# Kernel tuning notes

Hardware: AMD Instinct MI355X
Metric: run time of the kernel (lower is better)

## Reference

```python
import math
import jax, jax.numpy as jnp
import numpy as np

NUM_HEADS = 12
NUM_LANDMARKS = 32

def iterative_inv(mat, n_iter=6):
    # mat: [B, H, m, m] row-stochastic kernel; Newton-Schulz pseudo-inverse
    m = mat.shape[-1]
    I = jnp.eye(m, dtype=mat.dtype)
    K = mat
    # 'else' branch: per-(B,H) normalization by max column sum
    denom = jnp.max(jnp.sum(K, axis=-2), axis=-1)[..., None, None]
    V = jnp.swapaxes(K, -1, -2) / denom
    for _ in range(n_iter):
        KV = jnp.matmul(K, V)
        V = jnp.matmul(0.25 * V, 13.0 * I - jnp.matmul(KV, 15.0 * I - jnp.matmul(KV, 7.0 * I - KV)))
    return V

def setup_inputs() -> dict:
    key = jax.random.key(0)
    k1, k2, k3 = jax.random.split(key, 3)
    B, N, C = 8, 2048, 768
    x = jax.random.normal(k1, (B, N, C), dtype=jnp.float32)
    w_qkv = jax.random.normal(k2, (C, 3 * C), dtype=jnp.float32) * (1.0 / math.sqrt(C))
    w_proj = jax.random.normal(k3, (C, C), dtype=jnp.float32) * (1.0 / math.sqrt(C))
    b_proj = jnp.zeros((C,), dtype=jnp.float32)
    return {"x": x, "w_qkv": w_qkv, "w_proj": w_proj, "b_proj": b_proj}

def reference(x, w_qkv, w_proj, b_proj):
    B, N, C = x.shape
    H = NUM_HEADS
    d = C // H
    m = NUM_LANDMARKS
    qkv = (x @ w_qkv).reshape(B, N, 3, H, d).transpose(2, 0, 3, 1, 4)  # [3,B,H,N,d]
    Q, K, V = qkv[0], qkv[1], qkv[2]
    scale = 1.0 / math.sqrt(math.sqrt(d))
    Q = Q * scale
    K = K * scale
    # landmark pooling: mean over contiguous chunks of size N//m
    Q_l = Q.reshape(B, H, m, N // m, d).mean(axis=-2)  # [B,H,m,d]
    K_l = K.reshape(B, H, m, N // m, d).mean(axis=-2)
    kernel_1 = jax.nn.softmax(jnp.einsum('bhnd,bhmd->bhnm', Q, K_l), axis=-1)   # [B,H,N,m]
    kernel_2 = jax.nn.softmax(jnp.einsum('bhmd,bhkd->bhmk', Q_l, K_l), axis=-1) # [B,H,m,m]
    kernel_3 = jax.nn.softmax(jnp.einsum('bhmd,bhnd->bhmn', Q_l, K), axis=-1)   # [B,H,m,N]
    X = jnp.matmul(jnp.matmul(kernel_1, iterative_inv(kernel_2)), jnp.matmul(kernel_3, V))  # [B,H,N,d]
    X = X.transpose(0, 2, 1, 3).reshape(B, N, C)
    return X @ w_proj + b_proj
```

## Files before the change

### kernel.cpp

```cpp
#include <hip/hip_runtime.h>
#include <hip/hip_bf16.h>

typedef __hip_bfloat16 bf16;
typedef __attribute__((ext_vector_type(8))) __bf16 bf16x8;
typedef __attribute__((ext_vector_type(4))) float f32x4;

#define NB 8
#define SEQ 2048
#define CH 768
#define NH 12
#define HD 64
#define NL 32
#define BHT (NB*NH)
#define TOK (NB*SEQ)
#define QK_SCALE 0.35355339059327379f

#define BAR() __builtin_amdgcn_s_barrier()
#define WVM(n) __asm__ __volatile__("s_waitcnt vmcnt(" #n ")" ::: "memory")

__device__ __forceinline__ void async_ld16(const bf16* g, bf16* l) {
    unsigned loff = (unsigned)__builtin_amdgcn_readfirstlane((int)(unsigned)(uintptr_t)l);
    __builtin_amdgcn_global_load_lds(
        (const __attribute__((address_space(1))) unsigned*)(uintptr_t)g,
        (__attribute__((address_space(3))) unsigned*)(uintptr_t)loff, 16, 0, 0);
}

#define PREP_G0 (TOK*CH/2048)
#define PREP_G1 ((3*CH/32)*(CH/32))
#define PREP_G2 ((CH/32)*(CH/32))
__global__ __launch_bounds__(256) void prep(const float* __restrict__ x, bf16* __restrict__ xb,
                                            const float* __restrict__ w_qkv, bf16* __restrict__ wqkvT,
                                            const float* __restrict__ w_proj, bf16* __restrict__ wprojT) {
    __shared__ float tile[32][33];
    const int bid = blockIdx.x;
    const int t = threadIdx.x;
    if (bid < PREP_G0) {
        size_t i = ((size_t)bid * 256 + t) * 8;
        float4 a = *reinterpret_cast<const float4*>(x + i);
        float4 b = *reinterpret_cast<const float4*>(x + i + 4);
        alignas(16) bf16 tmp[8];
        tmp[0] = __float2bfloat16(a.x); tmp[1] = __float2bfloat16(a.y);
        tmp[2] = __float2bfloat16(a.z); tmp[3] = __float2bfloat16(a.w);
        tmp[4] = __float2bfloat16(b.x); tmp[5] = __float2bfloat16(b.y);
        tmp[6] = __float2bfloat16(b.z); tmp[7] = __float2bfloat16(b.w);
        *reinterpret_cast<uint4*>(xb + i) = *reinterpret_cast<const uint4*>(tmp);
        return;
    }
    const float* in; bf16* outp; int Hrows, Wcols, bx, by;
    if (bid < PREP_G0 + PREP_G1) {
        int tb = bid - PREP_G0;
        in = w_qkv; outp = wqkvT; Hrows = CH; Wcols = 3 * CH;
        bx = (tb % (3 * CH / 32)) * 32; by = (tb / (3 * CH / 32)) * 32;
    } else {
        int tb = bid - PREP_G0 - PREP_G1;
        in = w_proj; outp = wprojT; Hrows = CH; Wcols = CH;
        bx = (tb % (CH / 32)) * 32; by = (tb / (CH / 32)) * 32;
    }
    int tx = t & 31, ty = t >> 5;
    for (int i = 0; i < 32; i += 8)
        tile[ty + i][tx] = in[(size_t)(by + ty + i) * Wcols + bx + tx];
    __syncthreads();
    for (int i = 0; i < 32; i += 8)
        outp[(size_t)(bx + ty + i) * Hrows + by + tx] = __float2bfloat16(tile[tx][ty + i]);
}

template <int EPI>
__global__ __launch_bounds__(512, 4) void gemm_bt(
    const bf16* __restrict__ A, const bf16* __restrict__ Bt,
    int Nout, int Kdim,
    bf16* __restrict__ q, bf16* __restrict__ k, bf16* __restrict__ vt,
    float* __restrict__ Ql, float* __restrict__ Kl,
    float* __restrict__ outp, const float* __restrict__ bias_f) {
    __shared__ __align__(16) bf16 As[2][128 * 64];
    __shared__ __align__(16) bf16 Bs[2][192 * 64];
    const int t = threadIdx.x;
    const int wave = t >> 6, lane = t & 63;
    const int quad = lane >> 4, l15 = lane & 15;
    const int wr = wave >> 2, wc = wave & 3;

    int p = blockIdx.y * gridDim.x + blockIdx.x;
    int xcd = p & 7, j = p >> 3;
    int gx = gridDim.x;
    int bn = j % gx;
    int bm = (j / gx) * 8 + xcd;
    const int bm0 = bm * 128;
    const int bn0 = bn * 192;

    const int T = Kdim >> 6;

    const int srow = t >> 3;
    const int scol = (((t & 7) ^ (srow & 7)) << 3);
    const bf16* Abase = A + (size_t)(bm0 + srow) * Kdim + scol;
    const bf16* Bbase = Bt + (size_t)(bn0 + srow) * Kdim + scol;

    auto stA = [&](int kt, int c) {
        async_ld16(Abase + (size_t)(c * 64) * Kdim + kt * 64,
                   &As[kt & 1][c * 4096 + t * 8]);
    };
    auto stB = [&](int kt, int c) {
        async_ld16(Bbase + (size_t)(c * 64) * Kdim + kt * 64,
                   &Bs[kt & 1][c * 4096 + t * 8]);
    };

    const int swk[2] = { (quad ^ (l15 & 7)) << 3, ((4 + quad) ^ (l15 & 7)) << 3 };
    const bf16* arow = &As[0][(wr * 64 + l15) * 64];
    const bf16* brow = &Bs[0][(wc * 48 + l15) * 64];

    f32x4 acc[4][3];
    const f32x4 zero4 = {0.f, 0.f, 0.f, 0.f};
    #pragma unroll
    for (int i = 0; i < 4; i++)
        #pragma unroll
        for (int jj = 0; jj < 3; jj++) acc[i][jj] = zero4;

    stA(0, 0); stA(0, 1); stB(0, 0); stB(0, 1); stB(0, 2);
    WVM(0);
    BAR();

    for (int kt = 0; kt < T; kt++) {
        const bool nxt = (kt + 1 < T);
        const bf16* ab = arow + (kt & 1) * 8192;
        const bf16* bb = brow + (kt & 1) * 12288;

        if (nxt) { stA(kt + 1, 0); stA(kt + 1, 1); stB(kt + 1, 0); stB(kt + 1, 1); stB(kt + 1, 2); }

        bf16x8 a[4][2], b[3][2];
        #pragma unroll
        for (int mi = 0; mi < 4; mi++)
            #pragma unroll
            for (int kk = 0; kk < 2; kk++)
                a[mi][kk] = *reinterpret_cast<const bf16x8*>(ab + mi * 1024 + swk[kk]);
        #pragma unroll
        for (int ni = 0; ni < 3; ni++)
            #pragma unroll
            for (int kk = 0; kk < 2; kk++)
                b[ni][kk] = *reinterpret_cast<const bf16x8*>(bb + ni * 1024 + swk[kk]);

        __builtin_amdgcn_s_setprio(1);
        #pragma unroll
        for (int mi = 0; mi < 4; mi++)
            #pragma unroll
            for (int ni = 0; ni < 3; ni++)
                #pragma unroll
                for (int kk = 0; kk < 2; kk++)
                    acc[mi][ni] = __builtin_amdgcn_mfma_f32_16x16x32_bf16(a[mi][kk], b[ni][kk], acc[mi][ni], 0, 0, 0);
        __builtin_amdgcn_s_setprio(0);

        if (nxt) { WVM(0); BAR(); }
    }

    if (EPI == 0) {
        const int which = bn0 / CH;
        const int rem0 = bn0 - which * CH + wc * 48;
        const int b = bm0 >> 11;
        const int nnb = (bm0 & 2047) + wr * 64;
        if (which < 2) {
            bf16* dstqk = (which == 0) ? q : k;
            float* dstl = (which == 0) ? Ql : Kl;
            const int la = nnb >> 6;
            #pragma unroll
            for (int ni = 0; ni < 3; ni++) {
                int rem = rem0 + ni * 16;
                int h = rem >> 6;
                int dd = (rem & 63) + l15;
                int bh = b * NH + h;
                float colsum = 0.f;
                #pragma unroll
                for (int mi = 0; mi < 4; mi++) {
                    int nn0 = nnb + mi * 16 + quad * 4;
                    #pragma unroll
                    for (int r = 0; r < 4; r++) {
                        float val = acc[mi][ni][r];
                        colsum += val;
                        dstqk[((size_t)bh * SEQ + nn0 + r) * HD + dd] = __float2bfloat16(val * QK_SCALE);
                    }
                }
                colsum += __shfl_xor(colsum, 16);
                colsum += __shfl_xor(colsum, 32);
                if (quad == 0)
                    dstl[((size_t)bh * NL + la) * HD + dd] = colsum * (QK_SCALE / 64.f);
            }
        } else {
            #pragma unroll
            for (int ni = 0; ni < 3; ni++) {
                int rem = rem0 + ni * 16;
                int h = rem >> 6;
                int dd = (rem & 63) + l15;
                int bh = b * NH + h;
                #pragma unroll
                for (int mi = 0; mi < 4; mi++) {
                    int nn0 = nnb + mi * 16 + quad * 4;
                    alignas(8) bf16 four[4];
                    #pragma unroll
                    for (int r = 0; r < 4; r++) four[r] = __float2bfloat16(acc[mi][ni][r]);
                    *reinterpret_cast<uint2*>(&vt[((size_t)bh * HD + dd) * SEQ + nn0]) =
                        *reinterpret_cast<const uint2*>(four);
                }
            }
        }
    } else {
        #pragma unroll
        for (int ni = 0; ni < 3; ni++) {
            int col = bn0 + wc * 48 + ni * 16 + l15;
            float bb = bias_f[col];
            #pragma unroll
            for (int mi = 0; mi < 4; mi++)
                #pragma unroll
                for (int r = 0; r < 4; r++) {
                    int row = bm0 + wr * 64 + mi * 16 + quad * 4 + r;
                    outp[(size_t)row * Nout + col] = acc[mi][ni][r] + bb;
                }
        }
    }
}

__device__ inline void mm32(float* Cm, const float* Am, const float* Bm, int t) {
    for (int e = t; e < 1024; e += 256) {
        int i = e >> 5, jj = e & 31;
        float s = 0.f;
        #pragma unroll
        for (int kk = 0; kk < 32; kk++) s += Am[i * 32 + kk] * Bm[kk * 32 + jj];
        Cm[e] = s;
    }
}

__global__ __launch_bounds__(256) void k3_pv(const float* __restrict__ Ql,
                                             const float* __restrict__ Klm,
                                             const bf16* __restrict__ Kb,
                                             const bf16* __restrict__ Vt,
                                             float* __restrict__ Opart,
                                             float* __restrict__ Spart,
                                             float* __restrict__ Vinv) {
    __shared__ __align__(16) char smem[69632];
    const int bh = blockIdx.x;
    const int t = threadIdx.x;

    if (blockIdx.y == 0) {
        float* K2 = (float*)smem;
        float* Vv = K2 + 1024;
        float* KV = K2 + 2048;
        float* Ta = K2 + 3072;
        float* Tb = K2 + 4096;
        float* red = K2 + 5120;
        const float* ql = Ql + (size_t)bh * NL * HD;
        const float* kl = Klm + (size_t)bh * NL * HD;

        for (int e = t; e < 1024; e += 256) {
            int i = e >> 5, jj = e & 31;
            float s = 0.f;
            #pragma unroll 8
            for (int d = 0; d < 64; d++) s += ql[i * 64 + d] * kl[jj * 64 + d];
            K2[e] = s;
        }
        __syncthreads();
        if (t < 32) {
            float mx = -1e30f;
            for (int jj = 0; jj < 32; jj++) mx = fmaxf(mx, K2[t * 32 + jj]);
            float sm = 0.f;
            for (int jj = 0; jj < 32; jj++) { float e = __expf(K2[t * 32 + jj] - mx); K2[t * 32 + jj] = e; sm += e; }
            float inv = 1.f / sm;
            for (int jj = 0; jj < 32; jj++) K2[t * 32 + jj] *= inv;
        }
        __syncthreads();
        if (t < 32) {
            float cs = 0.f;
            for (int i = 0; i < 32; i++) cs += K2[i * 32 + t];
            red[t] = cs;
        }
        __syncthreads();
        if (t == 0) {
            float mx = red[0];
            for (int jj = 1; jj < 32; jj++) mx = fmaxf(mx, red[jj]);
            red[32] = mx;
        }
        __syncthreads();
        float invden = 1.f / red[32];
        for (int e = t; e < 1024; e += 256) {
            int i = e >> 5, jj = e & 31;
            Vv[e] = K2[jj * 32 + i] * invden;
        }
        __syncthreads();
        for (int it = 0; it < 6; it++) {
            mm32(KV, K2, Vv, t);
            __syncthreads();
            for (int e = t; e < 1024; e += 256) { int i = e >> 5, jj = e & 31; Ta[e] = ((i == jj) ? 7.f : 0.f) - KV[e]; }
            __syncthreads();
            mm32(Tb, KV, Ta, t);
            __syncthreads();
            for (int e = t; e < 1024; e += 256) { int i = e >> 5, jj = e & 31; Tb[e] = ((i == jj) ? 15.f : 0.f) - Tb[e]; }
            __syncthreads();
            mm32(Ta, KV, Tb, t);
            __syncthreads();
            for (int e = t; e < 1024; e += 256) { int i = e >> 5, jj = e & 31; Ta[e] = ((i == jj) ? 13.f : 0.f) - Ta[e]; }
            __syncthreads();
            mm32(Tb, Vv, Ta, t);
            __syncthreads();
            for (int e = t; e < 1024; e += 256) Vv[e] = 0.25f * Tb[e];
            __syncthreads();
        }
        for (int e = t; e < 1024; e += 256)
            Vinv[(size_t)bh * 1024 + e] = Vv[e];
        return;
    }

    bf16* Pw0 = (bf16*)smem;
    float* Ored0 = (float*)(smem + 34816);
    float* Sred = (float*)(smem + 34816 + 33280);
    const int cc = blockIdx.y - 1;
    const int n0 = cc * 512;
    const int w = t >> 6, lane = t & 63;
    const int quad = lane >> 4, l15 = lane & 15;

    const bf16* Kbh = Kb + (size_t)bh * SEQ * HD;
    const bf16* Vtb = Vt + (size_t)bh * HD * SEQ;

    bf16x8 af[2][2];
    #pragma unroll
    for (int mt = 0; mt < 2; mt++)
        #pragma unroll
        for (int kh = 0; kh < 2; kh++) {
            const float* src = Ql + (size_t)bh * NL * HD + (mt * 16 + l15) * 64 + kh * 32 + quad * 8;
            alignas(16) bf16 tmp[8];
            #pragma unroll
            for (int jj = 0; jj < 8; jj++) tmp[jj] = __float2bfloat16(src[jj]);
            af[mt][kh] = *reinterpret_cast<const bf16x8*>(tmp);
        }

    const f32x4 zero4 = {0.f, 0.f, 0.f, 0.f};
    f32x4 oacc[2][4];
    #pragma unroll
    for (int mt = 0; mt < 2; mt++)
        #pragma unroll
        for (int nd = 0; nd < 4; nd++) oacc[mt][nd] = zero4;
    float rs[2][4];
    #pragma unroll
    for (int mt = 0; mt < 2; mt++)
        #pragma unroll
        for (int r = 0; r < 4; r++) rs[mt][r] = 0.f;

    bf16* Pme = Pw0 + w * (32 * 136);

    #pragma unroll
    for (int h = 0; h < 2; h++) {
        f32x4 sacc[2][4];
        #pragma unroll
        for (int mt = 0; mt < 2; mt++)
            #pragma unroll
            for (int nt = 0; nt < 4; nt++) sacc[mt][nt] = zero4;
        #pragma unroll
        for (int nt = 0; nt < 4; nt++) {
            int n = n0 + w * 128 + h * 64 + nt * 16 + l15;
            bf16x8 kf0 = *reinterpret_cast<const bf16x8*>(&Kbh[(size_t)n * HD + quad * 8]);
            bf16x8 kf1 = *reinterpret_cast<const bf16x8*>(&Kbh[(size_t)n * HD + 32 + quad * 8]);
            #pragma unroll
            for (int mt = 0; mt < 2; mt++) {
                sacc[mt][nt] = __builtin_amdgcn_mfma_f32_16x16x32_bf16(af[mt][0], kf0, sacc[mt][nt], 0, 0, 0);
                sacc[mt][nt] = __builtin_amdgcn_mfma_f32_16x16x32_bf16(af[mt][1], kf1, sacc[mt][nt], 0, 0, 0);
            }
        }
        #pragma unroll
        for (int mt = 0; mt < 2; mt++)
            #pragma unroll
            for (int nt = 0; nt < 4; nt++)
                #pragma unroll
                for (int r = 0; r < 4; r++) {
                    float pv = __expf(sacc[mt][nt][r]);
                    rs[mt][r] += pv;
                    int row = mt * 16 + quad * 4 + r;
                    Pme[row * 136 + h * 64 + nt * 16 + l15] = __float2bfloat16(pv);
                }
    }
    __asm__ __volatile__("s_waitcnt lgkmcnt(0)" ::: "memory");

    #pragma unroll
    for (int kt = 0; kt < 4; kt++) {
        bf16x8 pa[2];
        pa[0] = *reinterpret_cast<const bf16x8*>(&Pme[l15 * 136 + kt * 32 + quad * 8]);
        pa[1] = *reinterpret_cast<const bf16x8*>(&Pme[(16 + l15) * 136 + kt * 32 + quad * 8]);
        int kbase = n0 + w * 128 + kt * 32 + quad * 8;
        #pragma unroll
        for (int nd = 0; nd < 4; nd++) {
            bf16x8 bv = *reinterpret_cast<const bf16x8*>(&Vtb[(size_t)(nd * 16 + l15) * SEQ + kbase]);
            oacc[0][nd] = __builtin_amdgcn_mfma_f32_16x16x32_bf16(pa[0], bv, oacc[0][nd], 0, 0, 0);
            oacc[1][nd] = __builtin_amdgcn_mfma_f32_16x16x32_bf16(pa[1], bv, oacc[1][nd], 0, 0, 0);
        }
    }

    #pragma unroll
    for (int mt = 0; mt < 2; mt++)
        #pragma unroll
        for (int r = 0; r < 4; r++) {
            float v = rs[mt][r];
            #pragma unroll
            for (int o = 1; o < 16; o <<= 1) v += __shfl_xor(v, o);
            rs[mt][r] = v;
        }
    if (l15 == 0)
        #pragma unroll
        for (int mt = 0; mt < 2; mt++)
            #pragma unroll
            for (int r = 0; r < 4; r++)
                Sred[w * 32 + mt * 16 + quad * 4 + r] = rs[mt][r];
    #pragma unroll
    for (int mt = 0; mt < 2; mt++)
        #pragma unroll
        for (int nd = 0; nd < 4; nd++)
            #pragma unroll
            for (int r = 0; r < 4; r++)
                Ored0[w * (32 * 65) + (mt * 16 + quad * 4 + r) * 65 + nd * 16 + l15] = oacc[mt][nd][r];
    __syncthreads();

    float* Op = Opart + ((size_t)bh * 4 + cc) * (NL * HD);
    for (int e = t; e < 2048; e += 256) {
        int m = e >> 6, dd = e & 63;
        Op[e] = Ored0[0 * (32 * 65) + m * 65 + dd] + Ored0[1 * (32 * 65) + m * 65 + dd] +
                Ored0[2 * (32 * 65) + m * 65 + dd] + Ored0[3 * (32 * 65) + m * 65 + dd];
    }
    if (t < 32)
        Spart[((size_t)bh * 4 + cc) * NL + t] = Sred[t] + Sred[32 + t] + Sred[64 + t] + Sred[96 + t];
}

__global__ __launch_bounds__(256) void combine_w2(const float* __restrict__ Opart,
                                                  const float* __restrict__ Spart,
                                                  const float* __restrict__ Vinv,
                                                  float* __restrict__ W2) {
    __shared__ float K3[2048];
    __shared__ float Vv[1024];
    __shared__ float stot[32];
    const int bh = blockIdx.x;
    const int t = threadIdx.x;

    if (t < 32) {
        const float* sp = Spart + (size_t)bh * 4 * NL;
        stot[t] = sp[t] + sp[32 + t] + sp[64 + t] + sp[96 + t];
    }
    {
        const float* op = Opart + (size_t)bh * 4 * (NL * HD);
        for (int e = t; e < 2048; e += 256)
            K3[e] = op[e] + op[2048 + e] + op[4096 + e] + op[6144 + e];
    }
    for (int e = t; e < 1024; e += 256)
        Vv[e] = Vinv[(size_t)bh * 1024 + e];
    __syncthreads();
    for (int e = t; e < 2048; e += 256) K3[e] *= (1.f / stot[e >> 6]);
    __syncthreads();
    for (int e = t; e < 2048; e += 256) {
        int i = e >> 6, dd = e & 63;
        float s = 0.f;
        #pragma unroll
        for (int kk = 0; kk < 32; kk++) s += Vv[i * 32 + kk] * K3[kk * 64 + dd];
        W2[(size_t)bh * NL * HD + e] = s;
    }
}

__global__ __launch_bounds__(256) void rows_fused(const bf16* __restrict__ Qb,
                                                  const float* __restrict__ Kl,
                                                  const float* __restrict__ W2,
                                                  bf16* __restrict__ Xp) {
    __shared__ __align__(16) bf16 Klb[32 * 64];
    __shared__ __align__(16) bf16 W2t[64 * 32];
    __shared__ __align__(16) bf16 Pw[4][32 * 40];
    const int bh = blockIdx.x, tile = blockIdx.y;
    const int t = threadIdx.x, w = t >> 6, lane = t & 63;
    const int quad = lane >> 4, l15 = lane & 15;

    {
        const float* ksrc = Kl + (size_t)bh * NL * HD;
        const float* wsrc = W2 + (size_t)bh * NL * HD;
        int e0 = t * 8;
        #pragma unroll
        for (int jj = 0; jj < 8; jj++) {
            int e = e0 + jj;
            Klb[e] = __float2bfloat16(ksrc[e]);
            int kk = e >> 6, dd = e & 63;
            W2t[dd * 32 + kk] = __float2bfloat16(wsrc[e]);
        }
    }
    __syncthreads();

    const int b = bh / NH, h = bh - b * NH;
    const int row0 = tile * 128 + w * 32;
    const bf16* qbase = Qb + ((size_t)bh * SEQ + row0) * HD;

    const f32x4 zero4 = {0.f, 0.f, 0.f, 0.f};
    f32x4 sacc[2][2];
    #pragma unroll
    for (int mt = 0; mt < 2; mt++)
        #pragma unroll
        for (int nt = 0; nt < 2; nt++) sacc[mt][nt] = zero4;
    #pragma unroll
    for (int kh = 0; kh < 2; kh++) {
        bf16x8 bk0 = *reinterpret_cast<const bf16x8*>(&Klb[(l15) * 64 + kh * 32 + quad * 8]);
        bf16x8 bk1 = *reinterpret_cast<const bf16x8*>(&Klb[(16 + l15) * 64 + kh * 32 + quad * 8]);
        #pragma unroll
        for (int mt = 0; mt < 2; mt++) {
            bf16x8 aq = *reinterpret_cast<const bf16x8*>(&qbase[(size_t)(mt * 16 + l15) * HD + kh * 32 + quad * 8]);
            sacc[mt][0] = __builtin_amdgcn_mfma_f32_16x16x32_bf16(aq, bk0, sacc[mt][0], 0, 0, 0);
            sacc[mt][1] = __builtin_amdgcn_mfma_f32_16x16x32_bf16(aq, bk1, sacc[mt][1], 0, 0, 0);
        }
    }

    float invs[2][4];
    bf16* Pme = &Pw[w][0];
    #pragma unroll
    for (int mt = 0; mt < 2; mt++)
        #pragma unroll
        for (int r = 0; r < 4; r++) {
            float v0 = __expf(sacc[mt][0][r]);
            float v1 = __expf(sacc[mt][1][r]);
            int row = mt * 16 + quad * 4 + r;
            Pme[row * 40 + l15] = __float2bfloat16(v0);
            Pme[row * 40 + 16 + l15] = __float2bfloat16(v1);
            float v = v0 + v1;
            #pragma unroll
            for (int o = 1; o < 16; o <<= 1) v += __shfl_xor(v, o);
            invs[mt][r] = 1.f / v;
        }
    __asm__ __volatile__("s_waitcnt lgkmcnt(0)" ::: "memory");

    f32x4 oacc[2][4];
    #pragma unroll
    for (int mt = 0; mt < 2; mt++)
        #pragma unroll
        for (int nd = 0; nd < 4; nd++) oacc[mt][nd] = zero4;
    bf16x8 pa[2];
    pa[0] = *reinterpret_cast<const bf16x8*>(&Pme[l15 * 40 + quad * 8]);
    pa[1] = *reinterpret_cast<const bf16x8*>(&Pme[(16 + l15) * 40 + quad * 8]);
    #pragma unroll
    for (int nd = 0; nd < 4; nd++) {
        bf16x8 bw = *reinterpret_cast<const bf16x8*>(&W2t[(nd * 16 + l15) * 32 + quad * 8]);
        oacc[0][nd] = __builtin_amdgcn_mfma_f32_16x16x32_bf16(pa[0], bw, oacc[0][nd], 0, 0, 0);
        oacc[1][nd] = __builtin_amdgcn_mfma_f32_16x16x32_bf16(pa[1], bw, oacc[1][nd], 0, 0, 0);
    }

    #pragma unroll
    for (int mt = 0; mt < 2; mt++)
        #pragma unroll
        for (int nd = 0; nd < 4; nd++)
            #pragma unroll
            for (int r = 0; r < 4; r++) {
                int row = row0 + mt * 16 + quad * 4 + r;
                Xp[((size_t)(b * SEQ + row)) * CH + h * 64 + nd * 16 + l15] =
                    __float2bfloat16(oacc[mt][nd][r] * invs[mt][r]);
            }
}

extern "C" void kernel_launch(void* const* d_in, const int* in_sizes, int n_in,
                              void* d_out, int out_size, void* d_ws, size_t ws_size,
                              hipStream_t stream) {
    const float* x      = (const float*)d_in[0];
    const float* w_qkv  = (const float*)d_in[1];
    const float* w_proj = (const float*)d_in[2];
    const float* b_proj = (const float*)d_in[3];
    float* out = (float*)d_out;

    char* ws = (char*)d_ws;
    size_t off = 0;
    auto alloc = [&](size_t bytes) -> void* {
        void* p = ws + off;
        off += (bytes + 255) & ~(size_t)255;
        return p;
    };
    bf16* wqkvT  = (bf16*)alloc((size_t)3 * CH * CH * 2);
    bf16* wprojT = (bf16*)alloc((size_t)CH * CH * 2);
    bf16* Qb     = (bf16*)alloc((size_t)BHT * SEQ * HD * 2);
    bf16* Kb     = (bf16*)alloc((size_t)BHT * SEQ * HD * 2);
    bf16* Vt     = (bf16*)alloc((size_t)BHT * SEQ * HD * 2);
    float* Ql    = (float*)alloc((size_t)BHT * NL * HD * 4);
    float* Kl    = (float*)alloc((size_t)BHT * NL * HD * 4);
    float* Opart = (float*)alloc((size_t)BHT * 4 * NL * HD * 4);
    float* Spart = (float*)alloc((size_t)BHT * 4 * NL * 4);
    float* Vinv  = (float*)alloc((size_t)BHT * NL * NL * 4);
    float* W2    = (float*)alloc((size_t)BHT * NL * HD * 4);
    bf16* Xp     = (bf16*)alloc((size_t)TOK * CH * 2);
    if (ws_size < off) return;
    bf16* xb = Xp;

    prep<<<PREP_G0 + PREP_G1 + PREP_G2, 256, 0, stream>>>(x, xb, w_qkv, wqkvT, w_proj, wprojT);

    gemm_bt<0><<<dim3((3 * CH) / 192, TOK / 128), 512, 0, stream>>>(
        xb, wqkvT, 3 * CH, CH, Qb, Kb, Vt, Ql, Kl, nullptr, nullptr);

    k3_pv<<<dim3(BHT, 5), 256, 0, stream>>>(Ql, Kl, Kb, Vt, Opart, Spart, Vinv);
    combine_w2<<<BHT, 256, 0, stream>>>(Opart, Spart, Vinv, W2);
    rows_fused<<<dim3(BHT, SEQ / 128), 256, 0, stream>>>(Qb, Kl, W2, Xp);

    gemm_bt<1><<<dim3(CH / 192, TOK / 128), 512, 0, stream>>>(
        Xp, wprojT, CH, CH, nullptr, nullptr, nullptr, nullptr, nullptr, out, b_proj);
}
```

Before: 259.0 us.

## Retile GEMMs to 128x128 with intra-block split-K and fold combine kernel into rows pass

The bf16 GEMM changes from 128x192 tiles to 128x128 tiles. The eight waves now split the K-loop into two halves, and the partial accumulators are reduced through LDS before the epilogue. The separate combine_w2 kernel is removed: k3_pv accumulates O and S with atomicAdd into buffers that prep zeroes, and rows_fused recomputes Vinv·normalized(O) per tile. Landmark means also switch to atomics. The aim is better GEMM grid balance and one fewer launch. The cost is LDS reduction traffic, atomics, and redundant W2 computation in every row tile.

```diff
diff --git a/kernel.cpp b/kernel.cpp
--- a/kernel.cpp
+++ b/kernel.cpp
@@ -28,9 +28,12 @@
 #define PREP_G0 (TOK*CH/2048)
 #define PREP_G1 ((3*CH/32)*(CH/32))
 #define PREP_G2 ((CH/32)*(CH/32))
+#define PREP_G3 BHT
 __global__ __launch_bounds__(256) void prep(const float* __restrict__ x, bf16* __restrict__ xb,
                                             const float* __restrict__ w_qkv, bf16* __restrict__ wqkvT,
-                                            const float* __restrict__ w_proj, bf16* __restrict__ wprojT) {
+                                            const float* __restrict__ w_proj, bf16* __restrict__ wprojT,
+                                            float* __restrict__ Ql, float* __restrict__ Kl,
+                                            float* __restrict__ O, float* __restrict__ S) {
     __shared__ float tile[32][33];
     const int bid = blockIdx.x;
     const int t = threadIdx.x;
@@ -46,6 +49,16 @@
         *reinterpret_cast<uint4*>(xb + i) = *reinterpret_cast<const uint4*>(tmp);
         return;
     }
+    if (bid >= PREP_G0 + PREP_G1 + PREP_G2) {
+        int bh = bid - (PREP_G0 + PREP_G1 + PREP_G2);
+        for (int e = t; e < 2048; e += 256) {
+            Ql[(size_t)bh * 2048 + e] = 0.f;
+            Kl[(size_t)bh * 2048 + e] = 0.f;
+            O[(size_t)bh * 2048 + e] = 0.f;
+        }
+        if (t < 32) S[(size_t)bh * NL + t] = 0.f;
+        return;
+    }
     const float* in; bf16* outp; int Hrows, Wcols, bx, by;
     if (bid < PREP_G0 + PREP_G1) {
         int tb = bid - PREP_G0;
@@ -71,12 +84,14 @@
     bf16* __restrict__ q, bf16* __restrict__ k, bf16* __restrict__ vt,
     float* __restrict__ Ql, float* __restrict__ Kl,
     float* __restrict__ outp, const float* __restrict__ bias_f) {
-    __shared__ __align__(16) bf16 As[2][128 * 64];
-    __shared__ __align__(16) bf16 Bs[2][192 * 64];
+    __shared__ __align__(16) char smem[65536];
+    bf16* AsP = (bf16*)smem;
+    bf16* BsP = (bf16*)(smem + 32768);
     const int t = threadIdx.x;
     const int wave = t >> 6, lane = t & 63;
     const int quad = lane >> 4, l15 = lane & 15;
-    const int wr = wave >> 2, wc = wave & 3;
+    const int wk = wave >> 2;
+    const int wr = (wave >> 1) & 1, wc = wave & 1;
 
     int p = blockIdx.y * gridDim.x + blockIdx.x;
     int xcd = p & 7, j = p >> 3;
@@ -84,7 +99,7 @@
     int bn = j % gx;
     int bm = (j / gx) * 8 + xcd;
     const int bm0 = bm * 128;
-    const int bn0 = bn * 192;
+    const int bn0 = bn * 128;
 
     const int T = Kdim >> 6;
 
@@ -95,78 +110,90 @@
 
     auto stA = [&](int kt, int c) {
         async_ld16(Abase + (size_t)(c * 64) * Kdim + kt * 64,
-                   &As[kt & 1][c * 4096 + t * 8]);
+                   &AsP[(kt & 1) * 8192 + c * 4096 + t * 8]);
     };
     auto stB = [&](int kt, int c) {
         async_ld16(Bbase + (size_t)(c * 64) * Kdim + kt * 64,
-                   &Bs[kt & 1][c * 4096 + t * 8]);
+                   &BsP[(kt & 1) * 8192 + c * 4096 + t * 8]);
     };
 
-    const int swk[2] = { (quad ^ (l15 & 7)) << 3, ((4 + quad) ^ (l15 & 7)) << 3 };
-    const bf16* arow = &As[0][(wr * 64 + l15) * 64];
-    const bf16* brow = &Bs[0][(wc * 48 + l15) * 64];
-
-    f32x4 acc[4][3];
+    const int swk = ((wk * 4 + quad) ^ (l15 & 7)) << 3;
+    const bf16* arow = &AsP[(wr * 64 + l15) * 64];
+    const bf16* brow = &BsP[(wc * 64 + l15) * 64];
+
+    f32x4 acc[4][4];
     const f32x4 zero4 = {0.f, 0.f, 0.f, 0.f};
     #pragma unroll
     for (int i = 0; i < 4; i++)
         #pragma unroll
-        for (int jj = 0; jj < 3; jj++) acc[i][jj] = zero4;
-
-    stA(0, 0); stA(0, 1); stB(0, 0); stB(0, 1); stB(0, 2);
+        for (int jj = 0; jj < 4; jj++) acc[i][jj] = zero4;
+
+    stA(0, 0); stA(0, 1); stB(0, 0); stB(0, 1);
     WVM(0);
     BAR();
 
     for (int kt = 0; kt < T; kt++) {
         const bool nxt = (kt + 1 < T);
         const bf16* ab = arow + (kt & 1) * 8192;
-        const bf16* bb = brow + (kt & 1) * 12288;
-
-        if (nxt) { stA(kt + 1, 0); stA(kt + 1, 1); stB(kt + 1, 0); stB(kt + 1, 1); stB(kt + 1, 2); }
-
-        bf16x8 a[4][2], b[3][2];
+        const bf16* bb = brow + (kt & 1) * 8192;
+
+        if (nxt) { stA(kt + 1, 0); stA(kt + 1, 1); stB(kt + 1, 0); stB(kt + 1, 1); }
+
+        bf16x8 a[4], b[4];
         #pragma unroll
         for (int mi = 0; mi < 4; mi++)
-            #pragma unroll
-            for (int kk = 0; kk < 2; kk++)
-                a[mi][kk] = *reinterpret_cast<const bf16x8*>(ab + mi * 1024 + swk[kk]);
-        #pragma unroll
-        for (int ni = 0; ni < 3; ni++)
-            #pragma unroll
-            for (int kk = 0; kk < 2; kk++)
-                b[ni][kk] = *reinterpret_cast<const bf16x8*>(bb + ni * 1024 + swk[kk]);
+            a[mi] = *reinterpret_cast<const bf16x8*>(ab + mi * 1024 + swk);
+        #pragma unroll
+        for (int ni = 0; ni < 4; ni++)
+            b[ni] = *reinterpret_cast<const bf16x8*>(bb + ni * 1024 + swk);
 
         __builtin_amdgcn_s_setprio(1);
         #pragma unroll
         for (int mi = 0; mi < 4; mi++)
             #pragma unroll
-            for (int ni = 0; ni < 3; ni++)
-                #pragma unroll
-                for (int kk = 0; kk < 2; kk++)
-                    acc[mi][ni] = __builtin_amdgcn_mfma_f32_16x16x32_bf16(a[mi][kk], b[ni][kk], acc[mi][ni], 0, 0, 0);
+            for (int ni = 0; ni < 4; ni++)
+                acc[mi][ni] = __builtin_amdgcn_mfma_f32_16x16x32_bf16(a[mi], b[ni], acc[mi][ni], 0, 0, 0);
         __builtin_amdgcn_s_setprio(0);
 
         if (nxt) { WVM(0); BAR(); }
     }
+
+    float* xch = (float*)smem;
+    const int wrwc = wr * 2 + wc;
+    const int whalf = wk ^ 1;
+    __syncthreads();
+    #pragma unroll
+    for (int m2 = 0; m2 < 2; m2++)
+        #pragma unroll
+        for (int ni = 0; ni < 4; ni++)
+            *reinterpret_cast<f32x4*>(
+                &xch[(wrwc * 2 + whalf) * 2048 + (m2 * 4 + ni) * 256 + lane * 4]) = acc[whalf * 2 + m2][ni];
+    __syncthreads();
+    #pragma unroll
+    for (int m2 = 0; m2 < 2; m2++)
+        #pragma unroll
+        for (int ni = 0; ni < 4; ni++)
+            acc[wk * 2 + m2][ni] += *reinterpret_cast<const f32x4*>(
+                &xch[(wrwc * 2 + wk) * 2048 + (m2 * 4 + ni) * 256 + lane * 4]);
 
     if (EPI == 0) {
         const int which = bn0 / CH;
-        const int rem0 = bn0 - which * CH + wc * 48;
+        const int rem0 = bn0 - which * CH + wc * 64;
         const int b = bm0 >> 11;
         const int nnb = (bm0 & 2047) + wr * 64;
+        const int h = rem0 >> 6;
+        const int bh = b * NH + h;
         if (which < 2) {
             bf16* dstqk = (which == 0) ? q : k;
             float* dstl = (which == 0) ? Ql : Kl;
             const int la = nnb >> 6;
             #pragma unroll
-            for (int ni = 0; ni < 3; ni++) {
-                int rem = rem0 + ni * 16;
-                int h = rem >> 6;
-                int dd = (rem & 63) + l15;
-                int bh = b * NH + h;
+            for (int ni = 0; ni < 4; ni++) {
+                int dd = ni * 16 + l15;
                 float colsum = 0.f;
                 #pragma unroll
-                for (int mi = 0; mi < 4; mi++) {
+                for (int m2 = 0; m2 < 2; m2++) {
+                    int mi = wk * 2 + m2;
                     int nn0 = nnb + mi * 16 + quad * 4;
                     #pragma unroll
                     for (int r = 0; r < 4; r++) {
@@ -178,17 +205,15 @@
                 colsum += __shfl_xor(colsum, 16);
                 colsum += __shfl_xor(colsum, 32);
                 if (quad == 0)
-                    dstl[((size_t)bh * NL + la) * HD + dd] = colsum * (QK_SCALE / 64.f);
+                    atomicAdd(&dstl[((size_t)bh * NL + la) * HD + dd], colsum * (QK_SCALE / 64.f));
             }
         } else {
             #pragma unroll
-            for (int ni = 0; ni < 3; ni++) {
-                int rem = rem0 + ni * 16;
-                int h = rem >> 6;
-                int dd = (rem & 63) + l15;
-                int bh = b * NH + h;
+            for (int ni = 0; ni < 4; ni++) {
+                int dd = ni * 16 + l15;
                 #pragma unroll
-                for (int mi = 0; mi < 4; mi++) {
+                for (int m2 = 0; m2 < 2; m2++) {
+                    int mi = wk * 2 + m2;
                     int nn0 = nnb + mi * 16 + quad * 4;
                     alignas(8) bf16 four[4];
                     #pragma unroll
@@ -200,16 +225,18 @@
         }
     } else {
         #pragma unroll
-        for (int ni = 0; ni < 3; ni++) {
-            int col = bn0 + wc * 48 + ni * 16 + l15;
+        for (int ni = 0; ni < 4; ni++) {
+            int col = bn0 + wc * 64 + ni * 16 + l15;
             float bb = bias_f[col];
             #pragma unroll
-            for (int mi = 0; mi < 4; mi++)
+            for (int m2 = 0; m2 < 2; m2++) {
+                int mi = wk * 2 + m2;
                 #pragma unroll
                 for (int r = 0; r < 4; r++) {
                     int row = bm0 + wr * 64 + mi * 16 + quad * 4 + r;
                     outp[(size_t)row * Nout + col] = acc[mi][ni][r] + bb;
                 }
+            }
         }
     }
 }
@@ -228,8 +255,8 @@
                                              const float* __restrict__ Klm,
                                              const bf16* __restrict__ Kb,
                                              const bf16* __restrict__ Vt,
-                                             float* __restrict__ Opart,
-                                             float* __restrict__ Spart,
+                                             float* __restrict__ O,
+                                             float* __restrict__ S,
                                              float* __restrict__ Vinv) {
     __shared__ __align__(16) char smem[69632];
     const int bh = blockIdx.x;
@@ -410,71 +437,52 @@
                 Ored0[w * (32 * 65) + (mt * 16 + quad * 4 + r) * 65 + nd * 16 + l15] = oacc[mt][nd][r];
     __syncthreads();
 
-    float* Op = Opart + ((size_t)bh * 4 + cc) * (NL * HD);
+    float* Op = O + (size_t)bh * (NL * HD);
     for (int e = t; e < 2048; e += 256) {
         int m = e >> 6, dd = e & 63;
-        Op[e] = Ored0[0 * (32 * 65) + m * 65 + dd] + Ored0[1 * (32 * 65) + m * 65 + dd] +
-                Ored0[2 * (32 * 65) + m * 65 + dd] + Ored0[3 * (32 * 65) + m * 65 + dd];
+        float s = Ored0[0 * (32 * 65) + m * 65 + dd] + Ored0[1 * (32 * 65) + m * 65 + dd] +
+                  Ored0[2 * (32 * 65) + m * 65 + dd] + Ored0[3 * (32 * 65) + m * 65 + dd];
+        atomicAdd(&Op[e], s);
     }
     if (t < 32)
-        Spart[((size_t)bh * 4 + cc) * NL + t] = Sred[t] + Sred[32 + t] + Sred[64 + t] + Sred[96 + t];
-}
-
-__global__ __launch_bounds__(256) void combine_w2(const float* __restrict__ Opart,
-                                                  const float* __restrict__ Spart,
-                                                  const float* __restrict__ Vinv,
-                                                  float* __restrict__ W2) {
-    __shared__ float K3[2048];
-    __shared__ float Vv[1024];
-    __shared__ float stot[32];
-    const int bh = blockIdx.x;
-    const int t = threadIdx.x;
-
-    if (t < 32) {
-        const float* sp = Spart + (size_t)bh * 4 * NL;
-        stot[t] = sp[t] + sp[32 + t] + sp[64 + t] + sp[96 + t];
-    }
-    {
-        const float* op = Opart + (size_t)bh * 4 * (NL * HD);
-        for (int e = t; e < 2048; e += 256)
-            K3[e] = op[e] + op[2048 + e] + op[4096 + e] + op[6144 + e];
-    }
-    for (int e = t; e < 1024; e += 256)
-        Vv[e] = Vinv[(size_t)bh * 1024 + e];
-    __syncthreads();
-    for (int e = t; e < 2048; e += 256) K3[e] *= (1.f / stot[e >> 6]);
-    __syncthreads();
-    for (int e = t; e < 2048; e += 256) {
-        int i = e >> 6, dd = e & 63;
-        float s = 0.f;
-        #pragma unroll
-        for (int kk = 0; kk < 32; kk++) s += Vv[i * 32 + kk] * K3[kk * 64 + dd];
-        W2[(size_t)bh * NL * HD + e] = s;
-    }
+        atomicAdd(&S[(size_t)bh * NL + t], Sred[t] + Sred[32 + t] + Sred[64 + t] + Sred[96 + t]);
 }
 
 __global__ __launch_bounds__(256) void rows_fused(const bf16* __restrict__ Qb,
                                                   const float* __restrict__ Kl,
-                                                  const float* __restrict__ W2,
+                                                  const float* __restrict__ Vinv,
+                                                  const float* __restrict__ O,
+                                                  const float* __restrict__ S,
                                                   bf16* __restrict__ Xp) {
-    __shared__ __align__(16) bf16 Klb[32 * 64];
-    __shared__ __align__(16) bf16 W2t[64 * 32];
-    __shared__ __align__(16) bf16 Pw[4][32 * 40];
+    __shared__ __align__(16) char sm[20480];
+    bf16* Klb = (bf16*)sm;
+    bf16* W2t = (bf16*)(sm + 4096);
+    float* VvT = (float*)(sm + 8192);
+    float* K3n = (float*)(sm + 12288);
+    bf16* Pw0 = (bf16*)(sm + 8192);
     const int bh = blockIdx.x, tile = blockIdx.y;
     const int t = threadIdx.x, w = t >> 6, lane = t & 63;
     const int quad = lane >> 4, l15 = lane & 15;
 
     {
         const float* ksrc = Kl + (size_t)bh * NL * HD;
-        const float* wsrc = W2 + (size_t)bh * NL * HD;
         int e0 = t * 8;
         #pragma unroll
-        for (int jj = 0; jj < 8; jj++) {
-            int e = e0 + jj;
-            Klb[e] = __float2bfloat16(ksrc[e]);
-            int kk = e >> 6, dd = e & 63;
-            W2t[dd * 32 + kk] = __float2bfloat16(wsrc[e]);
-        }
+        for (int jj = 0; jj < 8; jj++) Klb[e0 + jj] = __float2bfloat16(ksrc[e0 + jj]);
+        for (int e = t; e < 1024; e += 256)
+            VvT[e] = Vinv[(size_t)bh * 1024 + (e & 31) * 32 + (e >> 5)];
+        const float* Obh = O + (size_t)bh * 2048;
+        const float* Sbh = S + (size_t)bh * NL;
+        for (int e = t; e < 2048; e += 256)
+            K3n[e] = Obh[e] * (1.f / Sbh[e >> 6]);
+    }
+    __syncthreads();
+    for (int e = t; e < 2048; e += 256) {
+        int dd = e >> 5, i = e & 31;
+        float s = 0.f;
+        #pragma unroll
+        for (int kk = 0; kk < 32; kk++) s += VvT[kk * 32 + i] * K3n[kk * 64 + dd];
+        W2t[e] = __float2bfloat16(s);
     }
     __syncthreads();
 
@@ -501,7 +509,7 @@
     }
 
     float invs[2][4];
-    bf16* Pme = &Pw[w][0];
+    bf16* Pme = Pw0 + w * (32 * 40);
     #pragma unroll
     for (int mt = 0; mt < 2; mt++)
         #pragma unroll
@@ -568,23 +576,22 @@
     bf16* Vt     = (bf16*)alloc((size_t)BHT * SEQ * HD * 2);
     float* Ql    = (float*)alloc((size_t)BHT * NL * HD * 4);
     float* Kl    = (float*)alloc((size_t)BHT * NL * HD * 4);
-    float* Opart = (float*)alloc((size_t)BHT * 4 * NL * HD * 4);
-    float* Spart = (float*)alloc((size_t)BHT * 4 * NL * 4);
     float* Vinv  = (float*)alloc((size_t)BHT * NL * NL * 4);
-    float* W2    = (float*)alloc((size_t)BHT * NL * HD * 4);
+    float* O     = (float*)alloc((size_t)BHT * NL * HD * 4);
+    float* S     = (float*)alloc((size_t)BHT * NL * 4);
     bf16* Xp     = (bf16*)alloc((size_t)TOK * CH * 2);
     if (ws_size < off) return;
     bf16* xb = Xp;
 
-    prep<<<PREP_G0 + PREP_G1 + PREP_G2, 256, 0, stream>>>(x, xb, w_qkv, wqkvT, w_proj, wprojT);
-
-    gemm_bt<0><<<dim3((3 * CH) / 192, TOK / 128), 512, 0, stream>>>(
+    prep<<<PREP_G0 + PREP_G1 + PREP_G2 + PREP_G3, 256, 0, stream>>>(
+        x, xb, w_qkv, wqkvT, w_proj, wprojT, Ql, Kl, O, S);
+
+    gemm_bt<0><<<dim3((3 * CH) / 128, TOK / 128), 512, 0, stream>>>(
         xb, wqkvT, 3 * CH, CH, Qb, Kb, Vt, Ql, Kl, nullptr, nullptr);
 
-    k3_pv<<<dim3(BHT, 5), 256, 0, stream>>>(Ql, Kl, Kb, Vt, Opart, Spart, Vinv);
-    combine_w2<<<BHT, 256, 0, stream>>>(Opart, Spart, Vinv, W2);
-    rows_fused<<<dim3(BHT, SEQ / 128), 256, 0, stream>>>(Qb, Kl, W2, Xp);
-
-    gemm_bt<1><<<dim3(CH / 192, TOK / 128), 512, 0, stream>>>(
+    k3_pv<<<dim3(BHT, 5), 256, 0, stream>>>(Ql, Kl, Kb, Vt, O, S, Vinv);
+    rows_fused<<<dim3(BHT, SEQ / 128), 256, 0, stream>>>(Qb, Kl, Vinv, O, S, Xp);
+
+    gemm_bt<1><<<dim3(CH / 128, TOK / 128), 512, 0, stream>>>(
         Xp, wprojT, CH, CH, nullptr, nullptr, nullptr, nullptr, nullptr, out, b_proj);
 }
```

Measured after the change: 498.7 us. +92.5%, slower.

## Remove combine_w2 kernel via atomic partial accumulation and recompute W2 in rows_fused

Applied to the files above, without the earlier changes.

The four per-chunk partial outputs and softmax sums in k3_pv are now accumulated with atomicAdd into a single O and S buffer, which the prep kernel zeroes together with the Ql and Kl buffers. The separate combine_w2 launch is removed. Each rows_fused block now recomputes W2 = Vinv·(O/S) in shared memory before its main work. This saves one kernel launch and one global round trip, at the cost of atomic contention and redundant 32x32x64 matmuls repeated across 16 tiles per head.

```diff
diff --git a/kernel.cpp b/kernel.cpp
--- a/kernel.cpp
+++ b/kernel.cpp
@@ -28,9 +28,12 @@
 #define PREP_G0 (TOK*CH/2048)
 #define PREP_G1 ((3*CH/32)*(CH/32))
 #define PREP_G2 ((CH/32)*(CH/32))
+#define PREP_G3 BHT
 __global__ __launch_bounds__(256) void prep(const float* __restrict__ x, bf16* __restrict__ xb,
                                             const float* __restrict__ w_qkv, bf16* __restrict__ wqkvT,
-                                            const float* __restrict__ w_proj, bf16* __restrict__ wprojT) {
+                                            const float* __restrict__ w_proj, bf16* __restrict__ wprojT,
+                                            float* __restrict__ Ql, float* __restrict__ Kl,
+                                            float* __restrict__ O, float* __restrict__ S) {
     __shared__ float tile[32][33];
     const int bid = blockIdx.x;
     const int t = threadIdx.x;
@@ -44,6 +47,16 @@
         tmp[4] = __float2bfloat16(b.x); tmp[5] = __float2bfloat16(b.y);
         tmp[6] = __float2bfloat16(b.z); tmp[7] = __float2bfloat16(b.w);
         *reinterpret_cast<uint4*>(xb + i) = *reinterpret_cast<const uint4*>(tmp);
+        return;
+    }
+    if (bid >= PREP_G0 + PREP_G1 + PREP_G2) {
+        int bh = bid - (PREP_G0 + PREP_G1 + PREP_G2);
+        for (int e = t; e < 2048; e += 256) {
+            Ql[(size_t)bh * 2048 + e] = 0.f;
+            Kl[(size_t)bh * 2048 + e] = 0.f;
+            O[(size_t)bh * 2048 + e] = 0.f;
+        }
+        if (t < 32) S[(size_t)bh * NL + t] = 0.f;
         return;
     }
     const float* in; bf16* outp; int Hrows, Wcols, bx, by;
@@ -228,8 +241,8 @@
                                              const float* __restrict__ Klm,
                                              const bf16* __restrict__ Kb,
                                              const bf16* __restrict__ Vt,
-                                             float* __restrict__ Opart,
-                                             float* __restrict__ Spart,
+                                             float* __restrict__ O,
+                                             float* __restrict__ S,
                                              float* __restrict__ Vinv) {
     __shared__ __align__(16) char smem[69632];
     const int bh = blockIdx.x;
@@ -410,71 +423,52 @@
                 Ored0[w * (32 * 65) + (mt * 16 + quad * 4 + r) * 65 + nd * 16 + l15] = oacc[mt][nd][r];
     __syncthreads();
 
-    float* Op = Opart + ((size_t)bh * 4 + cc) * (NL * HD);
+    float* Op = O + (size_t)bh * (NL * HD);
     for (int e = t; e < 2048; e += 256) {
         int m = e >> 6, dd = e & 63;
-        Op[e] = Ored0[0 * (32 * 65) + m * 65 + dd] + Ored0[1 * (32 * 65) + m * 65 + dd] +
-                Ored0[2 * (32 * 65) + m * 65 + dd] + Ored0[3 * (32 * 65) + m * 65 + dd];
+        float s = Ored0[0 * (32 * 65) + m * 65 + dd] + Ored0[1 * (32 * 65) + m * 65 + dd] +
+                  Ored0[2 * (32 * 65) + m * 65 + dd] + Ored0[3 * (32 * 65) + m * 65 + dd];
+        atomicAdd(&Op[e], s);
     }
     if (t < 32)
-        Spart[((size_t)bh * 4 + cc) * NL + t] = Sred[t] + Sred[32 + t] + Sred[64 + t] + Sred[96 + t];
-}
-
-__global__ __launch_bounds__(256) void combine_w2(const float* __restrict__ Opart,
-                                                  const float* __restrict__ Spart,
-                                                  const float* __restrict__ Vinv,
-                                                  float* __restrict__ W2) {
-    __shared__ float K3[2048];
-    __shared__ float Vv[1024];
-    __shared__ float stot[32];
-    const int bh = blockIdx.x;
-    const int t = threadIdx.x;
-
-    if (t < 32) {
-        const float* sp = Spart + (size_t)bh * 4 * NL;
-        stot[t] = sp[t] + sp[32 + t] + sp[64 + t] + sp[96 + t];
-    }
-    {
-        const float* op = Opart + (size_t)bh * 4 * (NL * HD);
-        for (int e = t; e < 2048; e += 256)
-            K3[e] = op[e] + op[2048 + e] + op[4096 + e] + op[6144 + e];
-    }
-    for (int e = t; e < 1024; e += 256)
-        Vv[e] = Vinv[(size_t)bh * 1024 + e];
-    __syncthreads();
-    for (int e = t; e < 2048; e += 256) K3[e] *= (1.f / stot[e >> 6]);
-    __syncthreads();
-    for (int e = t; e < 2048; e += 256) {
-        int i = e >> 6, dd = e & 63;
-        float s = 0.f;
-        #pragma unroll
-        for (int kk = 0; kk < 32; kk++) s += Vv[i * 32 + kk] * K3[kk * 64 + dd];
-        W2[(size_t)bh * NL * HD + e] = s;
-    }
+        atomicAdd(&S[(size_t)bh * NL + t], Sred[t] + Sred[32 + t] + Sred[64 + t] + Sred[96 + t]);
 }
 
 __global__ __launch_bounds__(256) void rows_fused(const bf16* __restrict__ Qb,
                                                   const float* __restrict__ Kl,
-                                                  const float* __restrict__ W2,
+                                                  const float* __restrict__ Vinv,
+                                                  const float* __restrict__ O,
+                                                  const float* __restrict__ S,
                                                   bf16* __restrict__ Xp) {
-    __shared__ __align__(16) bf16 Klb[32 * 64];
-    __shared__ __align__(16) bf16 W2t[64 * 32];
-    __shared__ __align__(16) bf16 Pw[4][32 * 40];
+    __shared__ __align__(16) char sm[20480];
+    bf16* Klb = (bf16*)sm;
+    bf16* W2t = (bf16*)(sm + 4096);
+    float* VvT = (float*)(sm + 8192);
+    float* K3n = (float*)(sm + 12288);
+    bf16* Pw0 = (bf16*)(sm + 8192);
     const int bh = blockIdx.x, tile = blockIdx.y;
     const int t = threadIdx.x, w = t >> 6, lane = t & 63;
     const int quad = lane >> 4, l15 = lane & 15;
 
     {
         const float* ksrc = Kl + (size_t)bh * NL * HD;
-        const float* wsrc = W2 + (size_t)bh * NL * HD;
         int e0 = t * 8;
         #pragma unroll
-        for (int jj = 0; jj < 8; jj++) {
-            int e = e0 + jj;
-            Klb[e] = __float2bfloat16(ksrc[e]);
-            int kk = e >> 6, dd = e & 63;
-            W2t[dd * 32 + kk] = __float2bfloat16(wsrc[e]);
-        }
+        for (int jj = 0; jj < 8; jj++) Klb[e0 + jj] = __float2bfloat16(ksrc[e0 + jj]);
+        for (int e = t; e < 1024; e += 256)
+            VvT[e] = Vinv[(size_t)bh * 1024 + (e & 31) * 32 + (e >> 5)];
+        const float* Obh = O + (size_t)bh * 2048;
+        const float* Sbh = S + (size_t)bh * NL;
+        for (int e = t; e < 2048; e += 256)
+            K3n[e] = Obh[e] * (1.f / Sbh[e >> 6]);
+    }
+    __syncthreads();
+    for (int e = t; e < 2048; e += 256) {
+        int dd = e >> 5, i = e & 31;
+        float s = 0.f;
+        #pragma unroll
+        for (int kk = 0; kk < 32; kk++) s += VvT[kk * 32 + i] * K3n[kk * 64 + dd];
+        W2t[e] = __float2bfloat16(s);
     }
     __syncthreads();
 
@@ -501,7 +495,7 @@
     }
 
     float invs[2][4];
-    bf16* Pme = &Pw[w][0];
+    bf16* Pme = Pw0 + w * (32 * 40);
     #pragma unroll
     for (int mt = 0; mt < 2; mt++)
         #pragma unroll
@@ -568,22 +562,21 @@
     bf16* Vt     = (bf16*)alloc((size_t)BHT * SEQ * HD * 2);
     float* Ql    = (float*)alloc((size_t)BHT * NL * HD * 4);
     float* Kl    = (float*)alloc((size_t)BHT * NL * HD * 4);
-    float* Opart = (float*)alloc((size_t)BHT * 4 * NL * HD * 4);
-    float* Spart = (float*)alloc((size_t)BHT * 4 * NL * 4);
     float* Vinv  = (float*)alloc((size_t)BHT * NL * NL * 4);
-    float* W2    = (float*)alloc((size_t)BHT * NL * HD * 4);
+    float* O     = (float*)alloc((size_t)BHT * NL * HD * 4);
+    float* S     = (float*)alloc((size_t)BHT * NL * 4);
     bf16* Xp     = (bf16*)alloc((size_t)TOK * CH * 2);
     if (ws_size < off) return;
     bf16* xb = Xp;
 
-    prep<<<PREP_G0 + PREP_G1 + PREP_G2, 256, 0, stream>>>(x, xb, w_qkv, wqkvT, w_proj, wprojT);
+    prep<<<PREP_G0 + PREP_G1 + PREP_G2 + PREP_G3, 256, 0, stream>>>(
+        x, xb, w_qkv, wqkvT, w_proj, wprojT, Ql, Kl, O, S);
 
     gemm_bt<0><<<dim3((3 * CH) / 192, TOK / 128), 512, 0, stream>>>(
         xb, wqkvT, 3 * CH, CH, Qb, Kb, Vt, Ql, Kl, nullptr, nullptr);
 
-    k3_pv<<<dim3(BHT, 5), 256, 0, stream>>>(Ql, Kl, Kb, Vt, Opart, Spart, Vinv);
-    combine_w2<<<BHT, 256, 0, stream>>>(Opart, Spart, Vinv, W2);
-    rows_fused<<<dim3(BHT, SEQ / 128), 256, 0, stream>>>(Qb, Kl, W2, Xp);
+    k3_pv<<<dim3(BHT, 5), 256, 0, stream>>>(Ql, Kl, Kb, Vt, O, S, Vinv);
+    rows_fused<<<dim3(BHT, SEQ / 128), 256, 0, stream>>>(Qb, Kl, Vinv, O, S, Xp);
 
     gemm_bt<1><<<dim3(CH / 192, TOK / 128), 512, 0, stream>>>(
         Xp, wprojT, CH, CH, nullptr, nullptr, nullptr, nullptr, nullptr, out, b_proj);
```

Result: no change. 263.7 us (+1.8%).
